# Kernel optimization log

Measured on AMD Instinct MI355X. Metric: run time of the kernel, lower is better.

Reference implementation:

```python
import jax, jax.numpy as jnp
import numpy as np

NUM_USER = 100000
NUM_ENT = 100000
NUM_REL = 60
NUM_ITEM = 20000
ITEM_NUM_IN_KG = 20000
DIM = 64
N_NEIGHBOR = 8
N_ITER = 2
BATCH = 16384


def setup_inputs() -> dict:
    key = jax.random.key(0)
    ks = jax.random.split(key, 10)
    return {
        "u": jax.random.randint(ks[0], (BATCH,), 0, NUM_USER),
        "v": jax.random.randint(ks[1], (BATCH,), 0, NUM_ITEM),
        "usr_emb": jax.random.normal(ks[2], (NUM_USER, DIM), jnp.float32),
        "item_emb": jax.random.normal(ks[3], (NUM_ITEM, DIM), jnp.float32),
        "ent_emb": jax.random.normal(ks[4], (NUM_ENT + 1, DIM), jnp.float32),
        "rel_emb": jax.random.normal(ks[5], (NUM_REL + 1, DIM), jnp.float32),
        "W": jax.random.normal(ks[6], (DIM, DIM), jnp.float32) / np.sqrt(DIM),
        "b": jax.random.normal(ks[7], (DIM,), jnp.float32) * 0.01,
        "adj_ent": jax.random.randint(ks[8], (NUM_ENT + 1, N_NEIGHBOR), 0, NUM_ENT + 1),
        "adj_rel": jax.random.randint(ks[9], (NUM_ENT + 1, N_NEIGHBOR), 0, NUM_REL + 1),
    }


def reference(u, v, usr_emb, item_emb, ent_emb, rel_emb, W, b, adj_ent, adj_rel):
    B = u.shape[0]
    ue = usr_emb[u]  # [B, D]

    # hop-0 indices: items not in the KG map to the padding entity for neighbor lookup
    v_clip = jnp.where(v >= ITEM_NUM_IN_KG, NUM_ENT, v)
    ents = [v_clip[:, None]]  # [B, 1]
    rels = []
    for h in range(N_ITER):
        rels.append(adj_rel[ents[h]].reshape(B, -1))  # [B, 8**(h+1)]
        ents.append(adj_ent[ents[h]].reshape(B, -1))

    # hop-0 embedding uses the ORIGINAL v via the item table (entities[0][:] = v)
    ev = [item_emb[v[:, None]]] + [ent_emb[e] for e in ents[1:]]  # each [B, m, D]
    rv = [rel_emb[r] for r in rels]

    for i in range(N_ITER):
        act = jnp.tanh if i == N_ITER - 1 else jax.nn.sigmoid
        nxt = []
        for hop in range(N_ITER - i):
            sv = ev[hop]  # [B, m, D]
            m = sv.shape[1]
            nv = ev[hop + 1].reshape(B, m, N_NEIGHBOR, DIM)
            nr = rv[hop].reshape(B, m, N_NEIGHBOR, DIM)
            # user-relation attention over the 8 sampled neighbors
            scores = jnp.einsum("bd,bmnd->bmn", ue, nr)
            wgt = jax.nn.softmax(scores, axis=-1)
            agg = jnp.einsum("bmn,bmnd->bmd", wgt, nv)
            out = (sv + agg) @ W.T + b  # 'sum' aggregator
            nxt.append(act(out))
        ev = nxt

    item_vec = ev[0].reshape(B, DIM)
    return jax.nn.sigmoid(jnp.sum(ue * item_vec, axis=1))  # [B]
```

## Files before the change

### kernel.cpp

```cpp
#include <hip/hip_runtime.h>
#include <hip/hip_fp16.h>


namespace {

constexpr int kDim      = 64;
constexpr int kNN       = 8;
constexpr int kNumEnt   = 100000;
constexpr int kItemInKG = 20000;
constexpr int kElems    = 8;
constexpr int kRelChunks = 976;
constexpr int kP        = 72;
constexpr size_t kEntHalfBytes = (size_t)(kNumEnt + 1) * kDim * sizeof(__half);

typedef _Float16 f16x4 __attribute__((ext_vector_type(4)));
typedef _Float16 f16x8 __attribute__((ext_vector_type(8)));
typedef float    f32x4 __attribute__((ext_vector_type(4)));

__device__ __forceinline__ float fast_sigmoid(float x) {
  return 1.0f / (1.0f + __expf(-x));
}
__device__ __forceinline__ float fast_tanh(float x) {
  return 2.0f / (1.0f + __expf(-2.0f * x)) - 1.0f;
}
__device__ __forceinline__ float readlane_f(float v, int lane) {
  return __int_as_float(__builtin_amdgcn_readlane(__float_as_int(v), lane));
}
__device__ __forceinline__ f16x8 join8(f16x4 lo, f16x4 hi) {
  return __builtin_shufflevector(lo, hi, 0, 1, 2, 3, 4, 5, 6, 7);
}

__global__ void __launch_bounds__(256)
conv_kernel(const float* __restrict__ src, __half2* __restrict__ dst, int n4) {
  const int i = blockIdx.x * 256 + threadIdx.x;
  if (i < n4) {
    const float4 f = reinterpret_cast<const float4*>(src)[i];
    dst[2 * i + 0] = __floats2half2_rn(f.x, f.y);
    dst[2 * i + 1] = __floats2half2_rn(f.z, f.w);
  }
}

template <bool HALF>
__global__ void __launch_bounds__(kElems * 64)
__attribute__((amdgpu_waves_per_eu(4, 4)))
kgcn_kernel(const int* __restrict__ u, const int* __restrict__ v,
            const float* __restrict__ usr_emb, const float* __restrict__ item_emb,
            const float* __restrict__ ent_emb, const __half* __restrict__ ent_h,
            const float* __restrict__ rel_emb,
            const float* __restrict__ W, const float* __restrict__ bias,
            const int* __restrict__ adj_ent, const int* __restrict__ adj_rel,
            float* __restrict__ out)
{
  const int tid = threadIdx.x;
  const int wv  = tid >> 6;
  const int ln  = tid & 63;
  const int lq  = ln & 15;
  const int lg  = ln >> 4;
  const int b   = blockIdx.x * kElems + wv;

  __shared__ _Float16 s_wh[kDim * kP];
  __shared__ float    s_relt[kDim * 65];
  __shared__ _Float16 s_pre[80 * kP];
  __shared__ _Float16 s_h[72 * kP];
  __shared__ float    s_ue[kElems][kDim];

  const float4* W4 = reinterpret_cast<const float4*>(W);
  const float4* R4 = reinterpret_cast<const float4*>(rel_emb);
  const float4 wst0 = W4[tid];
  const float4 wst1 = W4[512 + tid];
  const float4 rst0 = R4[tid];
  const float4 rst1 = (512 + tid < kRelChunks) ? R4[512 + tid]
                                               : make_float4(0.f, 0.f, 0.f, 0.f);

  const int   uid = u[b];
  const int   vid = v[b];
  const float ue  = usr_emb[(size_t)uid * kDim + ln];
  const float ev0 = item_emb[(size_t)vid * kDim + ln];
  const int   e0  = (vid >= kItemInKG) ? kNumEnt : vid;

  int e1v = 0, r1v = 0;
  if (ln < kNN) {
    e1v = adj_ent[(size_t)e0 * kNN + ln];
    r1v = adj_rel[(size_t)e0 * kNN + ln];
  }
  const int parent = __shfl(e1v, ln >> 3, 64);
  const int e2v    = adj_ent[(size_t)parent * kNN + (ln & 7)];
  const int r2v    = adj_rel[(size_t)parent * kNN + (ln & 7)];

  {
    int id = tid, row = id >> 4, c4 = (id & 15) << 2;
    f16x4 h4;
    h4[0] = (_Float16)wst0.x; h4[1] = (_Float16)wst0.y;
    h4[2] = (_Float16)wst0.z; h4[3] = (_Float16)wst0.w;
    *reinterpret_cast<f16x4*>(&s_wh[row * kP + c4]) = h4;
    id = 512 + tid; row = id >> 4; c4 = (id & 15) << 2;
    f16x4 h5;
    h5[0] = (_Float16)wst1.x; h5[1] = (_Float16)wst1.y;
    h5[2] = (_Float16)wst1.z; h5[3] = (_Float16)wst1.w;
    *reinterpret_cast<f16x4*>(&s_wh[row * kP + c4]) = h5;
  }
  {
    int id = tid, r = id >> 4, c = (id & 15) << 2;
    s_relt[(c + 0) * 65 + r] = rst0.x;
    s_relt[(c + 1) * 65 + r] = rst0.y;
    s_relt[(c + 2) * 65 + r] = rst0.z;
    s_relt[(c + 3) * 65 + r] = rst0.w;
    id = 512 + tid; r = id >> 4; c = (id & 15) << 2;
    s_relt[(c + 0) * 65 + r] = rst1.x;
    s_relt[(c + 1) * 65 + r] = rst1.y;
    s_relt[(c + 2) * 65 + r] = rst1.z;
    s_relt[(c + 3) * 65 + r] = rst1.w;
  }
  s_ue[wv][ln] = ue;

  float ev1r[kNN];
  #pragma unroll
  for (int m = 0; m < kNN; ++m) {
    const size_t row = (size_t)__builtin_amdgcn_readlane(e1v, m) * kDim + ln;
    ev1r[m] = HALF ? __half2float(ent_h[row]) : ent_emb[row];
  }

  unsigned int g16[kDim];
  if constexpr (HALF) {
    const unsigned short* eh = reinterpret_cast<const unsigned short*>(ent_h);
    #pragma unroll
    for (int i = 0; i < kDim; ++i) {
      const size_t row = (size_t)__builtin_amdgcn_readlane(e2v, i) * kDim + ln;
      g16[i] = eh[row];
    }
  }

  __syncthreads();

  float t;
  {
    const float* relc = &s_relt[ln];
    float a0 = 0.f, a1 = 0.f, a2 = 0.f, a3 = 0.f;
    #pragma unroll
    for (int k = 0; k < kDim; k += 4) {
      a0 = fmaf(readlane_f(ue, k + 0), relc[(k + 0) * 65], a0);
      a1 = fmaf(readlane_f(ue, k + 1), relc[(k + 1) * 65], a1);
      a2 = fmaf(readlane_f(ue, k + 2), relc[(k + 2) * 65], a2);
      a3 = fmaf(readlane_f(ue, k + 3), relc[(k + 3) * 65], a3);
    }
    t = (a0 + a1) + (a2 + a3);
  }

  float w2v;
  {
    const float s2 = __shfl(t, r2v, 64);
    float mx = s2;
    #pragma unroll
    for (int m = 1; m <= 4; m <<= 1) mx = fmaxf(mx, __shfl_xor(mx, m, 64));
    const float e = __expf(s2 - mx);
    float sm = e;
    #pragma unroll
    for (int m = 1; m <= 4; m <<= 1) sm += __shfl_xor(sm, m, 64);
    w2v = e / sm;
  }
  float w0v;
  {
    const float s0 = __shfl(t, r1v, 64);
    float mx = s0;
    #pragma unroll
    for (int m = 1; m <= 4; m <<= 1) mx = fmaxf(mx, __shfl_xor(mx, m, 64));
    w0v = __expf(s0 - mx);
    float sm = w0v;
    #pragma unroll
    for (int m = 1; m <= 4; m <<= 1) sm += __shfl_xor(sm, m, 64);
    w0v /= sm;
  }

  if constexpr (HALF) {
    #pragma unroll
    for (int i = 0; i < kDim; ++i) asm volatile("" : "+v"(g16[i]));
  }

  {
    float agg = 0.f;
    #pragma unroll
    for (int n = 0; n < kNN; ++n)
      agg = fmaf(readlane_f(w0v, n), ev1r[n], agg);
    s_pre[(wv * 9 + 0) * kP + ln] = (_Float16)(ev0 + agg);
  }
  if constexpr (HALF) {
    #pragma unroll
    for (int m = 0; m < kNN; ++m) {
      float acc = 0.f;
      #pragma unroll
      for (int n = 0; n < kNN; ++n) {
        const float g = __half2float(
            __ushort_as_half((unsigned short)g16[m * kNN + n]));
        acc = fmaf(readlane_f(w2v, m * kNN + n), g, acc);
      }
      s_pre[(wv * 9 + 1 + m) * kP + ln] = (_Float16)(ev1r[m] + acc);
    }
  } else {
    #pragma unroll 2
    for (int m = 0; m < kNN; ++m) {
      float acc = 0.f;
      #pragma unroll
      for (int n = 0; n < kNN; ++n) {
        const size_t row =
            (size_t)__builtin_amdgcn_readlane(e2v, m * kNN + n) * kDim + ln;
        acc = fmaf(readlane_f(w2v, m * kNN + n), ent_emb[row], acc);
      }
      s_pre[(wv * 9 + 1 + m) * kP + ln] = (_Float16)(ev1r[m] + acc);
    }
  }

  float bcol[4];
  #pragma unroll
  for (int tt = 0; tt < 4; ++tt) bcol[tt] = bias[tt * 16 + lq];

  f16x8 Bf[8];
  #pragma unroll
  for (int tt = 0; tt < 4; ++tt) {
    #pragma unroll
    for (int s = 0; s < 2; ++s) {
      const _Float16* p = &s_wh[(tt * 16 + lq) * kP + s * 32 + lg * 4];
      Bf[tt * 2 + s] = join8(*reinterpret_cast<const f16x4*>(p),
                             *reinterpret_cast<const f16x4*>(p + 16));
    }
  }

  f16x8 Af[2];
  #pragma unroll
  for (int s = 0; s < 2; ++s) {
    const _Float16* p = &s_pre[(wv * 9 + lq) * kP + s * 32 + lg * 4];
    Af[s] = join8(*reinterpret_cast<const f16x4*>(p),
                  *reinterpret_cast<const f16x4*>(p + 16));
  }
  f32x4 acc[4];
  #pragma unroll
  for (int tt = 0; tt < 4; ++tt) acc[tt] = f32x4{0.f, 0.f, 0.f, 0.f};
  #pragma unroll
  for (int tt = 0; tt < 4; ++tt)
    #pragma unroll
    for (int s = 0; s < 2; ++s)
      acc[tt] = __builtin_amdgcn_mfma_f32_16x16x32_f16(Af[s], Bf[tt * 2 + s],
                                                       acc[tt], 0, 0, 0);

  #pragma unroll
  for (int tt = 0; tt < 4; ++tt) {
    #pragma unroll
    for (int r = 0; r < 4; ++r) {
      const int vec = lg * 4 + r;
      if (vec < 9)
        s_h[(wv * 9 + vec) * kP + tt * 16 + lq] =
            (_Float16)fast_sigmoid(acc[tt][r] + bcol[tt]);
    }
  }

  {
    float pre = (float)s_h[(wv * 9 + 0) * kP + ln];
    #pragma unroll
    for (int n = 0; n < kNN; ++n)
      pre = fmaf(readlane_f(w0v, n), (float)s_h[(wv * 9 + 1 + n) * kP + ln],
                 pre);
    s_pre[(wv * 9 + 0) * kP + ln] = (_Float16)pre;
  }

  f16x8 Ff[2];
  #pragma unroll
  for (int s = 0; s < 2; ++s) {
    const _Float16* p = &s_pre[(wv * 9 + 0) * kP + s * 32 + lg * 4];
    Ff[s] = join8(*reinterpret_cast<const f16x4*>(p),
                  *reinterpret_cast<const f16x4*>(p + 16));
  }
  f32x4 fa[4];
  #pragma unroll
  for (int tt = 0; tt < 4; ++tt) fa[tt] = f32x4{0.f, 0.f, 0.f, 0.f};
  #pragma unroll
  for (int tt = 0; tt < 4; ++tt)
    #pragma unroll
    for (int s = 0; s < 2; ++s)
      fa[tt] = __builtin_amdgcn_mfma_f32_16x16x32_f16(Ff[s], Bf[tt * 2 + s],
                                                      fa[tt], 0, 0, 0);

  float part = 0.f;
  if (ln < 16) {
    #pragma unroll
    for (int tt = 0; tt < 4; ++tt) {
      const float item = fast_tanh(fa[tt][0] + bcol[tt]);
      part = fmaf(item, s_ue[wv][tt * 16 + ln], part);
    }
  }
  #pragma unroll
  for (int off = 1; off <= 8; off <<= 1)
    part += __shfl_xor(part, off, 64);
  if (ln == 0) out[b] = fast_sigmoid(part);
}

}

extern "C" void kernel_launch(void* const* d_in, const int* in_sizes, int n_in,
                              void* d_out, int out_size, void* d_ws, size_t ws_size,
                              hipStream_t stream) {
  const int*   u        = (const int*)d_in[0];
  const int*   v        = (const int*)d_in[1];
  const float* usr_emb  = (const float*)d_in[2];
  const float* item_emb = (const float*)d_in[3];
  const float* ent_emb  = (const float*)d_in[4];
  const float* rel_emb  = (const float*)d_in[5];
  const float* W        = (const float*)d_in[6];
  const float* bias     = (const float*)d_in[7];
  const int*   adj_ent  = (const int*)d_in[8];
  const int*   adj_rel  = (const int*)d_in[9];
  float*       out      = (float*)d_out;

  const int B = in_sizes[0];
  dim3 grid(B / kElems), block(kElems * 64);

  const bool use_half = (ws_size >= kEntHalfBytes);
  if (use_half) {
    __half* ent_h = (__half*)d_ws;
    const int n4 = (kNumEnt + 1) * kDim / 4;
    hipLaunchKernelGGL(conv_kernel, dim3((n4 + 255) / 256), dim3(256), 0,
                       stream, ent_emb, (__half2*)ent_h, n4);
    hipLaunchKernelGGL((kgcn_kernel<true>), grid, block, 0, stream,
                       u, v, usr_emb, item_emb, ent_emb, ent_h, rel_emb, W,
                       bias, adj_ent, adj_rel, out);
  } else {
    hipLaunchKernelGGL((kgcn_kernel<false>), grid, block, 0, stream,
                       u, v, usr_emb, item_emb, ent_emb, (const __half*)d_ws,
                       rel_emb, W, bias, adj_ent, adj_rel, out);
  }
}
```

Before: 53.38 us.

## Compute user-relation scores with MFMA and shrink shared memory footprint

Replaces the scalar readlane/FMA loop over a transposed fp32 relation table with an fp16 MFMA that multiplies the user vector by the relation embeddings. Scores are then fetched by relation id through cross-lane shuffles. Shared memory is also reduced: the row pitch drops from 72 to 68, s_pre is smaller, and relations and the user vector are stored in fp16. The waves_per_eu upper bound is removed, and the final dot product is reworked into a full-wave reduction using the in-register user value. This adds fp16 rounding of relation and user embeddings in the attention scores and needs extra shuffles for each lookup.

```diff
diff --git a/kernel.cpp b/kernel.cpp
--- a/kernel.cpp
+++ b/kernel.cpp
@@ -10,7 +10,7 @@
 constexpr int kItemInKG = 20000;
 constexpr int kElems    = 8;
 constexpr int kRelChunks = 976;
-constexpr int kP        = 72;
+constexpr int kP        = 68;
 constexpr size_t kEntHalfBytes = (size_t)(kNumEnt + 1) * kDim * sizeof(__half);
 
 typedef _Float16 f16x4 __attribute__((ext_vector_type(4)));
@@ -28,6 +28,12 @@
 }
 __device__ __forceinline__ f16x8 join8(f16x4 lo, f16x4 hi) {
   return __builtin_shufflevector(lo, hi, 0, 1, 2, 3, 4, 5, 6, 7);
+}
+__device__ __forceinline__ f16x4 cvt4(float4 f) {
+  f16x4 h;
+  h[0] = (_Float16)f.x; h[1] = (_Float16)f.y;
+  h[2] = (_Float16)f.z; h[3] = (_Float16)f.w;
+  return h;
 }
 
 __global__ void __launch_bounds__(256)
@@ -42,7 +48,7 @@
 
 template <bool HALF>
 __global__ void __launch_bounds__(kElems * 64)
-__attribute__((amdgpu_waves_per_eu(4, 4)))
+__attribute__((amdgpu_waves_per_eu(4)))
 kgcn_kernel(const int* __restrict__ u, const int* __restrict__ v,
             const float* __restrict__ usr_emb, const float* __restrict__ item_emb,
             const float* __restrict__ ent_emb, const __half* __restrict__ ent_h,
@@ -58,11 +64,11 @@
   const int lg  = ln >> 4;
   const int b   = blockIdx.x * kElems + wv;
 
-  __shared__ _Float16 s_wh[kDim * kP];
-  __shared__ float    s_relt[kDim * 65];
-  __shared__ _Float16 s_pre[80 * kP];
-  __shared__ _Float16 s_h[72 * kP];
-  __shared__ float    s_ue[kElems][kDim];
+  __shared__ __align__(16) _Float16 s_wh[kDim * kP];
+  __shared__ __align__(16) _Float16 s_relh[kDim * kP];
+  __shared__ __align__(16) _Float16 s_ueh[kElems * kDim];
+  __shared__ __align__(16) _Float16 s_pre[72 * kP];
+  __shared__ __align__(16) _Float16 s_h[72 * kP];
 
   const float4* W4 = reinterpret_cast<const float4*>(W);
   const float4* R4 = reinterpret_cast<const float4*>(rel_emb);
@@ -89,29 +95,13 @@
 
   {
     int id = tid, row = id >> 4, c4 = (id & 15) << 2;
-    f16x4 h4;
-    h4[0] = (_Float16)wst0.x; h4[1] = (_Float16)wst0.y;
-    h4[2] = (_Float16)wst0.z; h4[3] = (_Float16)wst0.w;
-    *reinterpret_cast<f16x4*>(&s_wh[row * kP + c4]) = h4;
+    *reinterpret_cast<f16x4*>(&s_wh[row * kP + c4]) = cvt4(wst0);
+    *reinterpret_cast<f16x4*>(&s_relh[row * kP + c4]) = cvt4(rst0);
     id = 512 + tid; row = id >> 4; c4 = (id & 15) << 2;
-    f16x4 h5;
-    h5[0] = (_Float16)wst1.x; h5[1] = (_Float16)wst1.y;
-    h5[2] = (_Float16)wst1.z; h5[3] = (_Float16)wst1.w;
-    *reinterpret_cast<f16x4*>(&s_wh[row * kP + c4]) = h5;
-  }
-  {
-    int id = tid, r = id >> 4, c = (id & 15) << 2;
-    s_relt[(c + 0) * 65 + r] = rst0.x;
-    s_relt[(c + 1) * 65 + r] = rst0.y;
-    s_relt[(c + 2) * 65 + r] = rst0.z;
-    s_relt[(c + 3) * 65 + r] = rst0.w;
-    id = 512 + tid; r = id >> 4; c = (id & 15) << 2;
-    s_relt[(c + 0) * 65 + r] = rst1.x;
-    s_relt[(c + 1) * 65 + r] = rst1.y;
-    s_relt[(c + 2) * 65 + r] = rst1.z;
-    s_relt[(c + 3) * 65 + r] = rst1.w;
-  }
-  s_ue[wv][ln] = ue;
+    *reinterpret_cast<f16x4*>(&s_wh[row * kP + c4]) = cvt4(wst1);
+    *reinterpret_cast<f16x4*>(&s_relh[row * kP + c4]) = cvt4(rst1);
+  }
+  s_ueh[wv * kDim + ln] = (_Float16)ue;
 
   float ev1r[kNN];
   #pragma unroll
@@ -132,23 +122,40 @@
 
   __syncthreads();
 
-  float t;
-  {
-    const float* relc = &s_relt[ln];
-    float a0 = 0.f, a1 = 0.f, a2 = 0.f, a3 = 0.f;
-    #pragma unroll
-    for (int k = 0; k < kDim; k += 4) {
-      a0 = fmaf(readlane_f(ue, k + 0), relc[(k + 0) * 65], a0);
-      a1 = fmaf(readlane_f(ue, k + 1), relc[(k + 1) * 65], a1);
-      a2 = fmaf(readlane_f(ue, k + 2), relc[(k + 2) * 65], a2);
-      a3 = fmaf(readlane_f(ue, k + 3), relc[(k + 3) * 65], a3);
-    }
-    t = (a0 + a1) + (a2 + a3);
-  }
+  f16x8 Au[2];
+  #pragma unroll
+  for (int s = 0; s < 2; ++s) {
+    const _Float16* p = &s_ueh[wv * kDim + s * 32 + lg * 4];
+    Au[s] = join8(*reinterpret_cast<const f16x4*>(p),
+                  *reinterpret_cast<const f16x4*>(p + 16));
+  }
+  f32x4 ts[4];
+  #pragma unroll
+  for (int tt = 0; tt < 4; ++tt) {
+    ts[tt] = f32x4{0.f, 0.f, 0.f, 0.f};
+    #pragma unroll
+    for (int s = 0; s < 2; ++s) {
+      const _Float16* p = &s_relh[(tt * 16 + lq) * kP + s * 32 + lg * 4];
+      const f16x8 Rf = join8(*reinterpret_cast<const f16x4*>(p),
+                             *reinterpret_cast<const f16x4*>(p + 16));
+      ts[tt] = __builtin_amdgcn_mfma_f32_16x16x32_f16(Au[s], Rf, ts[tt],
+                                                      0, 0, 0);
+    }
+  }
+  auto t_lookup = [&](int r) -> float {
+    const int sl = r & 15;
+    const float c0 = __shfl(ts[0][0], sl, 64);
+    const float c1 = __shfl(ts[1][0], sl, 64);
+    const float c2 = __shfl(ts[2][0], sl, 64);
+    const float c3 = __shfl(ts[3][0], sl, 64);
+    const float ab = (r & 16) ? c1 : c0;
+    const float cd = (r & 16) ? c3 : c2;
+    return (r & 32) ? cd : ab;
+  };
 
   float w2v;
   {
-    const float s2 = __shfl(t, r2v, 64);
+    const float s2 = t_lookup(r2v);
     float mx = s2;
     #pragma unroll
     for (int m = 1; m <= 4; m <<= 1) mx = fmaxf(mx, __shfl_xor(mx, m, 64));
@@ -160,7 +167,7 @@
   }
   float w0v;
   {
-    const float s0 = __shfl(t, r1v, 64);
+    const float s0 = t_lookup(r1v);
     float mx = s0;
     #pragma unroll
     for (int m = 1; m <= 4; m <<= 1) mx = fmaxf(mx, __shfl_xor(mx, m, 64));
@@ -224,10 +231,11 @@
     }
   }
 
+  const int arow = wv * 9 + (lq < 9 ? lq : 8);
   f16x8 Af[2];
   #pragma unroll
   for (int s = 0; s < 2; ++s) {
-    const _Float16* p = &s_pre[(wv * 9 + lq) * kP + s * 32 + lg * 4];
+    const _Float16* p = &s_pre[arow * kP + s * 32 + lg * 4];
     Af[s] = join8(*reinterpret_cast<const f16x4*>(p),
                   *reinterpret_cast<const f16x4*>(p + 16));
   }
@@ -278,18 +286,17 @@
       fa[tt] = __builtin_amdgcn_mfma_f32_16x16x32_f16(Ff[s], Bf[tt * 2 + s],
                                                       fa[tt], 0, 0, 0);
 
-  float part = 0.f;
-  if (ln < 16) {
-    #pragma unroll
-    for (int tt = 0; tt < 4; ++tt) {
-      const float item = fast_tanh(fa[tt][0] + bcol[tt]);
-      part = fmaf(item, s_ue[wv][tt * 16 + ln], part);
-    }
-  }
-  #pragma unroll
-  for (int off = 1; off <= 8; off <<= 1)
-    part += __shfl_xor(part, off, 64);
-  if (ln == 0) out[b] = fast_sigmoid(part);
+  {
+    float fown = fa[0][0], bown = bcol[0];
+    if (lg == 1) { fown = fa[1][0]; bown = bcol[1]; }
+    if (lg == 2) { fown = fa[2][0]; bown = bcol[2]; }
+    if (lg == 3) { fown = fa[3][0]; bown = bcol[3]; }
+    float part = fast_tanh(fown + bown) * ue;
+    #pragma unroll
+    for (int off = 32; off > 0; off >>= 1)
+      part += __shfl_xor(part, off, 64);
+    if (ln == 0) out[b] = fast_sigmoid(part);
+  }
 }
 
 }
```

New measurement: 52.38 us. About the same (-1.9%).
